# Optimization experiments

Measured on AMD Instinct MI355X. Metric: run time of the kernel, lower is better.

The kernel has to match this reference:

```python
import jax, jax.numpy as jnp
import numpy as np

WS = 7          # window_size
NH = 12         # num_heads
EPS = 1e-5      # LayerNorm eps


def setup_inputs() -> dict:
    key = jax.random.key(0)
    ks = jax.random.split(key, 8)
    B, H, W, C = 32, 56, 56, 384
    x = jax.random.normal(ks[0], (B, H * W, C), dtype=jnp.float32)
    s = 1.0 / np.sqrt(C)
    return {
        "x": x,
        "ln_gamma": jnp.ones((C,), jnp.float32),
        "ln_beta": jnp.zeros((C,), jnp.float32),
        "w_in": jax.random.normal(ks[1], (3 * C, C), jnp.float32) * s,   # torch in_proj_weight
        "b_in": jnp.zeros((3 * C,), jnp.float32),
        "w_out": jax.random.normal(ks[2], (C, C), jnp.float32) * s,      # torch out_proj.weight
        "b_out": jnp.zeros((C,), jnp.float32),
        "H": H,
        "W": W,
    }


def reference(x, ln_gamma, ln_beta, w_in, b_in, w_out, b_out, H, W):
    B, N, C = x.shape
    assert N == H * W
    hd = C // NH
    shortcut = x

    # LayerNorm
    mu = jnp.mean(x, axis=-1, keepdims=True)
    var = jnp.mean((x - mu) ** 2, axis=-1, keepdims=True)
    y = (x - mu) * jax.lax.rsqrt(var + EPS) * ln_gamma + ln_beta

    # window partition (pads are static Python ints)
    y = y.reshape(B, H, W, C)
    pad_h = (WS - H % WS) % WS
    pad_w = (WS - W % WS) % WS
    y = jnp.pad(y, ((0, 0), (0, pad_h), (0, pad_w), (0, 0)))
    Hp, Wp = H + pad_h, W + pad_w
    nh, nw = Hp // WS, Wp // WS
    y = y.reshape(B, nh, WS, nw, WS, C).transpose(0, 1, 3, 2, 4, 5)
    y = y.reshape(B * nh * nw, WS * WS, C)   # [NWIN, L, C]

    # MHA (torch nn.MultiheadAttention, batch_first)
    qkv = y @ w_in.T + b_in                   # [NWIN, L, 3C]
    q, k, v = jnp.split(qkv, 3, axis=-1)
    NWIN, L, _ = y.shape
    q = q.reshape(NWIN, L, NH, hd).transpose(0, 2, 1, 3)
    k = k.reshape(NWIN, L, NH, hd).transpose(0, 2, 1, 3)
    v = v.reshape(NWIN, L, NH, hd).transpose(0, 2, 1, 3)
    scores = jnp.einsum("whqd,whkd->whqk", q, k) / jnp.sqrt(jnp.float32(hd))
    attn = jax.nn.softmax(scores, axis=-1)
    o = jnp.einsum("whqk,whkd->whqd", attn, v)
    o = o.transpose(0, 2, 1, 3).reshape(NWIN, L, C)
    o = o @ w_out.T + b_out

    # window reverse + unpad + residual
    o = o.reshape(B, nh, nw, WS, WS, C).transpose(0, 1, 3, 2, 4, 5)
    o = o.reshape(B, Hp, Wp, C)[:, :H, :W, :].reshape(B, N, C)
    return shortcut + o
```

## Files before the change

### kernel.cpp

```cpp
#include <hip/hip_runtime.h>

typedef __bf16 bf16x8 __attribute__((ext_vector_type(8)));
typedef float f32x4 __attribute__((ext_vector_type(4)));
typedef unsigned short ushort8 __attribute__((ext_vector_type(8)));
typedef unsigned int uu2 __attribute__((ext_vector_type(2)));

#define LDS_AS(p) ((__attribute__((address_space(3))) void*)(p))
#define GLB_AS(p) ((const __attribute__((address_space(1))) void*)(p))

__device__ __forceinline__ unsigned short f2bf(float f) {
    union { float f; unsigned u; } v; v.f = f;
    unsigned r = v.u + 0x7fffu + ((v.u >> 16) & 1u);
    return (unsigned short)(r >> 16);
}

__global__ __launch_bounds__(256) void convw_kernel(
    const float* __restrict__ wi, const float* __restrict__ wo,
    unsigned short* __restrict__ qw, unsigned short* __restrict__ ow)
{
    const int i = blockIdx.x * 256 + threadIdx.x;
    if (i < 1152 * 384) qw[i] = f2bf(wi[i]);
    if (i < 384 * 384)  ow[i] = f2bf(wo[i]);
}

__global__ __launch_bounds__(256) void ln_kernel(
    const float* __restrict__ x, const float* __restrict__ gam,
    const float* __restrict__ bet, unsigned short* __restrict__ y)
{
    const int lane = threadIdx.x & 63;
    const int wv   = threadIdx.x >> 6;
    const int m    = blockIdx.x * 4 + wv;
    const int win  = m / 49, l = m - win * 49;
    const int b = win >> 6, wh = (win >> 3) & 7, ww = win & 7;
    const int i = l / 7, j = l - i * 7;
    const float2* xr = (const float2*)(x + ((size_t)b * 3136 + (wh * 7 + i) * 56 + (ww * 7 + j)) * 384);

    float2 v[3];
    float s = 0.f, ss = 0.f;
#pragma unroll
    for (int t = 0; t < 3; ++t) {
        v[t] = xr[t * 64 + lane];
        s  += v[t].x + v[t].y;
        ss += v[t].x * v[t].x + v[t].y * v[t].y;
    }
#pragma unroll
    for (int d = 1; d < 64; d <<= 1) {
        s  += __shfl_xor(s, d, 64);
        ss += __shfl_xor(ss, d, 64);
    }
    const float mu  = s * (1.f / 384.f);
    const float var = ss * (1.f / 384.f) - mu * mu;
    const float rs  = rsqrtf(var + 1e-5f);

    unsigned* yr = (unsigned*)(y + (size_t)m * 384);
#pragma unroll
    for (int t = 0; t < 3; ++t) {
        const int c = (t * 64 + lane) * 2;
        float a0 = (v[t].x - mu) * rs * gam[c]     + bet[c];
        float a1 = (v[t].y - mu) * rs * gam[c + 1] + bet[c + 1];
        yr[t * 64 + lane] = (unsigned)f2bf(a0) | ((unsigned)f2bf(a1) << 16);
    }
}

template <int N_, int EPI>
__global__ __launch_bounds__(256) void gemm_kernel(
    const unsigned short* __restrict__ A,
    const unsigned short* __restrict__ Bw,
    const float* __restrict__ bias,
    unsigned short* __restrict__ obf,
    const float* __restrict__ xres,
    float* __restrict__ oflt)
{
    __shared__ unsigned short As[2][128 * 32];
    __shared__ unsigned short Bs[2][128 * 32];
    const int lane = threadIdx.x & 63;
    const int wv   = threadIdx.x >> 6;

    const int NB = N_ / 128;
    int sw = blockIdx.x;
    if ((gridDim.x & 7) == 0)
        sw = (sw & 7) * (int)(gridDim.x >> 3) + (sw >> 3);
    const int my = sw / NB;
    const int m0 = my * 128;
    const int n0 = (sw - my * NB) * 128;

    const int wm = (wv & 1) * 64;
    const int wn = (wv >> 1) * 64;
    const int cl = lane & 15;
    const int qd = lane >> 4;
    const int srow = wv * 16 + (lane >> 2);
    const int scol = (lane & 3) * 8;

    f32x4 acc[4][4] = {};

#define STAGE(BUF, KB) do {                                                                              \
    const unsigned short* ga = A  + (size_t)(m0 + srow) * 384 + (KB) * 32 + scol;                        \
    const unsigned short* gb = Bw + (size_t)(n0 + srow) * 384 + (KB) * 32 + scol;                        \
    __builtin_amdgcn_global_load_lds(GLB_AS(ga),            LDS_AS(&As[BUF][(wv * 16) * 32]),        16, 0, 0); \
    __builtin_amdgcn_global_load_lds(GLB_AS(ga + 64 * 384), LDS_AS(&As[BUF][(64 + wv * 16) * 32]),   16, 0, 0); \
    __builtin_amdgcn_global_load_lds(GLB_AS(gb),            LDS_AS(&Bs[BUF][(wv * 16) * 32]),        16, 0, 0); \
    __builtin_amdgcn_global_load_lds(GLB_AS(gb + 64 * 384), LDS_AS(&Bs[BUF][(64 + wv * 16) * 32]),   16, 0, 0); \
  } while (0)

    STAGE(0, 0);
    __syncthreads();

#pragma unroll
    for (int kb = 0; kb < 12; ++kb) {
        const int cur = kb & 1;
        if (kb < 11) STAGE(cur ^ 1, kb + 1);

        bf16x8 af[4], bfr[4];
#pragma unroll
        for (int mt = 0; mt < 4; ++mt)
            af[mt] = *(const bf16x8*)(&As[cur][(wm + mt * 16 + cl) * 32 + qd * 8]);
#pragma unroll
        for (int nt = 0; nt < 4; ++nt)
            bfr[nt] = *(const bf16x8*)(&Bs[cur][(wn + nt * 16 + cl) * 32 + qd * 8]);
#pragma unroll
        for (int mt = 0; mt < 4; ++mt)
#pragma unroll
            for (int nt = 0; nt < 4; ++nt)
                acc[mt][nt] = __builtin_amdgcn_mfma_f32_16x16x32_bf16(bfr[nt], af[mt], acc[mt][nt], 0, 0, 0);

        __syncthreads();
    }
#undef STAGE

#pragma unroll
    for (int mt = 0; mt < 4; ++mt) {
        const int m = m0 + wm + mt * 16 + cl;
        size_t rowbase = 0;
        if (EPI == 1) {
            const int win = m / 49, l = m - win * 49;
            const int b = win >> 6, wh = (win >> 3) & 7, ww = win & 7;
            const int i = l / 7, j = l - i * 7;
            rowbase = ((size_t)b * 3136 + (wh * 7 + i) * 56 + (ww * 7 + j)) * 384;
        }
#pragma unroll
        for (int nt = 0; nt < 4; ++nt) {
            const int nb = n0 + wn + nt * 16 + qd * 4;
            const f32x4 bv = *(const f32x4*)(bias + nb);
            if (EPI == 0) {
                uu2 p;
                p[0] = (unsigned)f2bf(acc[mt][nt][0] + bv[0]) |
                       ((unsigned)f2bf(acc[mt][nt][1] + bv[1]) << 16);
                p[1] = (unsigned)f2bf(acc[mt][nt][2] + bv[2]) |
                       ((unsigned)f2bf(acc[mt][nt][3] + bv[3]) << 16);
                *(uu2*)(obf + (size_t)m * N_ + nb) = p;
            } else {
                const f32x4 xr = *(const f32x4*)(xres + rowbase + nb);
                f32x4 o;
#pragma unroll
                for (int r = 0; r < 4; ++r) o[r] = acc[mt][nt][r] + bv[r] + xr[r];
                *(f32x4*)(oflt + rowbase + nb) = o;
            }
        }
    }
}

__global__ __launch_bounds__(256) void attn_kernel(
    const unsigned short* __restrict__ qkv, unsigned short* __restrict__ o)
{
    __shared__ unsigned short P[4][64 * 72];
    const int lane = threadIdx.x & 63;
    const int wv   = threadIdx.x >> 6;
    const int cl = lane & 15;
    const int qd = lane >> 4;
    const int g   = blockIdx.x * 4 + wv;
    const int win = g / 12;
    const int h   = g - win * 12;
    const unsigned short* base = qkv + (size_t)win * (49 * 1152);

    bf16x8 aq[4], bk[4];
#pragma unroll
    for (int mt = 0; mt < 4; ++mt) {
        const int l = mt * 16 + cl;
        bf16x8 z = {};
        if (l < 49) z = *(const bf16x8*)(base + (size_t)l * 1152 + h * 32 + qd * 8);
        aq[mt] = z;
    }
#pragma unroll
    for (int nt = 0; nt < 4; ++nt) {
        const int lk = nt * 16 + cl;
        bf16x8 z = {};
        if (lk < 49) z = *(const bf16x8*)(base + (size_t)lk * 1152 + 384 + h * 32 + qd * 8);
        bk[nt] = z;
    }
    f32x4 s[4][4] = {};
#pragma unroll
    for (int mt = 0; mt < 4; ++mt)
#pragma unroll
        for (int nt = 0; nt < 4; ++nt)
            s[mt][nt] = __builtin_amdgcn_mfma_f32_16x16x32_bf16(aq[mt], bk[nt], s[mt][nt], 0, 0, 0);

    const float scale = 0.17677669529663687f;
#pragma unroll
    for (int mt = 0; mt < 4; ++mt)
#pragma unroll
        for (int nt = 0; nt < 4; ++nt)
#pragma unroll
            for (int r = 0; r < 4; ++r) {
                float t = s[mt][nt][r] * scale;
                if (nt * 16 + cl >= 49) t = -1e30f;
                s[mt][nt][r] = t;
            }

#pragma unroll
    for (int mt = 0; mt < 4; ++mt)
#pragma unroll
        for (int r = 0; r < 4; ++r) {
            float mx = fmaxf(fmaxf(s[mt][0][r], s[mt][1][r]), fmaxf(s[mt][2][r], s[mt][3][r]));
            mx = fmaxf(mx, __shfl_xor(mx, 1, 64));
            mx = fmaxf(mx, __shfl_xor(mx, 2, 64));
            mx = fmaxf(mx, __shfl_xor(mx, 4, 64));
            mx = fmaxf(mx, __shfl_xor(mx, 8, 64));
            float sm = 0.f;
#pragma unroll
            for (int nt = 0; nt < 4; ++nt) {
                const float p = __expf(s[mt][nt][r] - mx);
                s[mt][nt][r] = p;
                sm += p;
            }
            sm += __shfl_xor(sm, 1, 64);
            sm += __shfl_xor(sm, 2, 64);
            sm += __shfl_xor(sm, 4, 64);
            sm += __shfl_xor(sm, 8, 64);
            const float inv = 1.f / sm;
#pragma unroll
            for (int nt = 0; nt < 4; ++nt)
                s[mt][nt][r] *= inv;
        }

    unsigned short* Pw = &P[wv][0];
#pragma unroll
    for (int mt = 0; mt < 4; ++mt)
#pragma unroll
        for (int nt = 0; nt < 4; ++nt)
#pragma unroll
            for (int r = 0; r < 4; ++r)
                Pw[(mt * 16 + qd * 4 + r) * 72 + nt * 16 + cl] = f2bf(s[mt][nt][r]);

    f32x4 oa[4][2] = {};
    const unsigned short* vbase = base + 768 + h * 32;
#pragma unroll
    for (int kk = 0; kk < 2; ++kk) {
        bf16x8 ap[4];
#pragma unroll
        for (int mt = 0; mt < 4; ++mt)
            ap[mt] = *(const bf16x8*)(Pw + (mt * 16 + cl) * 72 + kk * 32 + qd * 8);
#pragma unroll
        for (int nt = 0; nt < 2; ++nt) {
            ushort8 tv;
#pragma unroll
            for (int jj = 0; jj < 8; ++jj) {
                const int lk = kk * 32 + qd * 8 + jj;
                tv[jj] = (lk < 49) ? vbase[(size_t)lk * 1152 + nt * 16 + cl] : (unsigned short)0;
            }
            const bf16x8 bv = __builtin_bit_cast(bf16x8, tv);
#pragma unroll
            for (int mt = 0; mt < 4; ++mt)
                oa[mt][nt] = __builtin_amdgcn_mfma_f32_16x16x32_bf16(ap[mt], bv, oa[mt][nt], 0, 0, 0);
        }
    }

    unsigned short* ob = o + (size_t)win * 49 * 384 + h * 32;
#pragma unroll
    for (int mt = 0; mt < 4; ++mt)
#pragma unroll
        for (int r = 0; r < 4; ++r) {
            const int l = mt * 16 + qd * 4 + r;
            if (l < 49) {
#pragma unroll
                for (int nt = 0; nt < 2; ++nt)
                    ob[(size_t)l * 384 + nt * 16 + cl] = f2bf(oa[mt][nt][r]);
            }
        }
}

extern "C" void kernel_launch(void* const* d_in, const int* in_sizes, int n_in,
                              void* d_out, int out_size, void* d_ws, size_t ws_size,
                              hipStream_t stream)
{
    const float* x   = (const float*)d_in[0];
    const float* gam = (const float*)d_in[1];
    const float* bet = (const float*)d_in[2];
    const float* wi  = (const float*)d_in[3];
    const float* bi  = (const float*)d_in[4];
    const float* wo  = (const float*)d_in[5];
    const float* bo  = (const float*)d_in[6];
    float* out = (float*)d_out;

    const int Bb   = in_sizes[0] / (3136 * 384);
    const int M    = Bb * 3136;
    const int NWIN = Bb * 64;

    char* ws = (char*)d_ws;
    unsigned short* qw   = (unsigned short*)(ws);
    unsigned short* ow   = (unsigned short*)(ws + 884736);
    unsigned short* y    = (unsigned short*)(ws + 1179648);
    unsigned short* qkv  = (unsigned short*)(ws + 1179648 + (size_t)M * 768);
    unsigned short* owin = (unsigned short*)(ws + 1179648 + (size_t)M * 768 + (size_t)M * 2304);

    convw_kernel<<<1728, 256, 0, stream>>>(wi, wo, qw, ow);
    ln_kernel<<<M / 4, 256, 0, stream>>>(x, gam, bet, y);
    gemm_kernel<1152, 0><<<(M / 128) * 9, 256, 0, stream>>>(y, qw, bi, qkv, nullptr, nullptr);
    attn_kernel<<<NWIN * 12 / 4, 256, 0, stream>>>(qkv, owin);
    gemm_kernel<384, 1><<<(M / 128) * 3, 256, 0, stream>>>(owin, ow, bo, nullptr, x, out);
}
```

Before: 646.5 us.

## Restructure GEMM into 256x128 tiles with 8 waves, K=64 stages and XOR-swizzled LDS

The GEMM block tile grows to 256x128 with 512 threads (8 waves) and K-step 64, and LDS is XOR-swizzled to avoid bank conflicts. Global-to-LDS loads for the next stage are split across four sub-phases, interleaved with MFMA groups, and separated by manual s_waitcnt/s_barrier plus setprio hints. The aim is better overlap of memory and compute and fewer barriers per unit of K. In exchange the kernel uses more LDS and more registers, and the hand-written waitcnt counts risk races if the compiler reorders memory operations. It also assumes M is divisible by 256; M = 100352 = 392*256, so that holds here.

Result: slower. 696.4 us (+7.7%).

```diff
diff --git a/kernel.cpp b/kernel.cpp
--- a/kernel.cpp
+++ b/kernel.cpp
@@ -63,7 +63,7 @@
 }
 
 template <int N_, int EPI>
-__global__ __launch_bounds__(256) void gemm_kernel(
+__global__ __launch_bounds__(512, 2) void gemm_kernel(
     const unsigned short* __restrict__ A,
     const unsigned short* __restrict__ Bw,
     const float* __restrict__ bias,
@@ -71,8 +71,8 @@
     const float* __restrict__ xres,
     float* __restrict__ oflt)
 {
-    __shared__ unsigned short As[2][128 * 32];
-    __shared__ unsigned short Bs[2][128 * 32];
+    __shared__ unsigned short As[2][256 * 64];
+    __shared__ unsigned short Bs[2][128 * 64];
     const int lane = threadIdx.x & 63;
     const int wv   = threadIdx.x >> 6;
 
@@ -81,51 +81,100 @@
     if ((gridDim.x & 7) == 0)
         sw = (sw & 7) * (int)(gridDim.x >> 3) + (sw >> 3);
     const int my = sw / NB;
-    const int m0 = my * 128;
+    const int m0 = my * 256;
     const int n0 = (sw - my * NB) * 128;
 
-    const int wm = (wv & 1) * 64;
-    const int wn = (wv >> 1) * 64;
+    const int wm = (wv & 3) * 64;
+    const int wn = (wv >> 2) * 64;
     const int cl = lane & 15;
     const int qd = lane >> 4;
-    const int srow = wv * 16 + (lane >> 2);
-    const int scol = (lane & 3) * 8;
+    const int rc0 = ((qd ^ (cl & 7)) * 8);
+
+    const int srow  = lane >> 3;
+    const int sperm = ((lane & 7) ^ srow) * 8;
+
+    const unsigned short* gA = A  + (size_t)(m0 + wv * 32 + srow) * 384 + sperm;
+    const unsigned short* gB = Bw + (size_t)(n0 + wv * 16 + srow) * 384 + sperm;
 
     f32x4 acc[4][4] = {};
 
-#define STAGE(BUF, KB) do {                                                                              \
-    const unsigned short* ga = A  + (size_t)(m0 + srow) * 384 + (KB) * 32 + scol;                        \
-    const unsigned short* gb = Bw + (size_t)(n0 + srow) * 384 + (KB) * 32 + scol;                        \
-    __builtin_amdgcn_global_load_lds(GLB_AS(ga),            LDS_AS(&As[BUF][(wv * 16) * 32]),        16, 0, 0); \
-    __builtin_amdgcn_global_load_lds(GLB_AS(ga + 64 * 384), LDS_AS(&As[BUF][(64 + wv * 16) * 32]),   16, 0, 0); \
-    __builtin_amdgcn_global_load_lds(GLB_AS(gb),            LDS_AS(&Bs[BUF][(wv * 16) * 32]),        16, 0, 0); \
-    __builtin_amdgcn_global_load_lds(GLB_AS(gb + 64 * 384), LDS_AS(&Bs[BUF][(64 + wv * 16) * 32]),   16, 0, 0); \
-  } while (0)
-
-    STAGE(0, 0);
-    __syncthreads();
-
-#pragma unroll
-    for (int kb = 0; kb < 12; ++kb) {
+#define GLA(BUF, KT, I) __builtin_amdgcn_global_load_lds(GLB_AS(gA + (I) * 8 * 384 + (KT) * 64), \
+                            LDS_AS(&As[BUF][(wv * 32 + (I) * 8) * 64]), 16, 0, 0)
+#define GLB_(BUF, KT, I) __builtin_amdgcn_global_load_lds(GLB_AS(gB + (I) * 8 * 384 + (KT) * 64), \
+                            LDS_AS(&Bs[BUF][(wv * 16 + (I) * 8) * 64]), 16, 0, 0)
+#define LDA(row, off) (*(const bf16x8*)(Ac + (row) * 64 + (off)))
+#define LDB(row, off) (*(const bf16x8*)(Bc + (row) * 64 + (off)))
+
+    GLA(0, 0, 0); GLA(0, 0, 1); GLA(0, 0, 2); GLA(0, 0, 3);
+    GLB_(0, 0, 0); GLB_(0, 0, 1);
+
+#pragma unroll
+    for (int kb = 0; kb < 6; ++kb) {
         const int cur = kb & 1;
-        if (kb < 11) STAGE(cur ^ 1, kb + 1);
-
-        bf16x8 af[4], bfr[4];
-#pragma unroll
-        for (int mt = 0; mt < 4; ++mt)
-            af[mt] = *(const bf16x8*)(&As[cur][(wm + mt * 16 + cl) * 32 + qd * 8]);
-#pragma unroll
-        for (int nt = 0; nt < 4; ++nt)
-            bfr[nt] = *(const bf16x8*)(&Bs[cur][(wn + nt * 16 + cl) * 32 + qd * 8]);
-#pragma unroll
-        for (int mt = 0; mt < 4; ++mt)
-#pragma unroll
-            for (int nt = 0; nt < 4; ++nt)
-                acc[mt][nt] = __builtin_amdgcn_mfma_f32_16x16x32_bf16(bfr[nt], af[mt], acc[mt][nt], 0, 0, 0);
-
-        __syncthreads();
-    }
-#undef STAGE
+        const int nxt = cur ^ 1;
+
+        if (kb < 5) {
+            GLA(nxt, kb + 1, 0); GLA(nxt, kb + 1, 1);
+            asm volatile("s_waitcnt vmcnt(2)\n\ts_barrier" ::: "memory");
+        } else {
+            asm volatile("s_waitcnt vmcnt(0)\n\ts_barrier" ::: "memory");
+        }
+
+        const unsigned short* Ac = &As[cur][0];
+        const unsigned short* Bc = &Bs[cur][0];
+        const int rc1 = rc0 ^ 32;
+        bf16x8 af0, af1, bf[4];
+
+        af0 = LDA(wm + cl,      rc0);
+        af1 = LDA(wm + 16 + cl, rc0);
+#pragma unroll
+        for (int nt = 0; nt < 4; ++nt) bf[nt] = LDB(wn + nt * 16 + cl, rc0);
+        __builtin_amdgcn_s_setprio(1);
+#pragma unroll
+        for (int nt = 0; nt < 4; ++nt) acc[0][nt] = __builtin_amdgcn_mfma_f32_16x16x32_bf16(bf[nt], af0, acc[0][nt], 0, 0, 0);
+#pragma unroll
+        for (int nt = 0; nt < 4; ++nt) acc[1][nt] = __builtin_amdgcn_mfma_f32_16x16x32_bf16(bf[nt], af1, acc[1][nt], 0, 0, 0);
+        __builtin_amdgcn_s_setprio(0);
+        asm volatile("s_barrier" ::: "memory");
+
+        af0 = LDA(wm + 32 + cl, rc0);
+        af1 = LDA(wm + 48 + cl, rc0);
+        if (kb < 5) { GLA(nxt, kb + 1, 2); GLA(nxt, kb + 1, 3); }
+        __builtin_amdgcn_s_setprio(1);
+#pragma unroll
+        for (int nt = 0; nt < 4; ++nt) acc[2][nt] = __builtin_amdgcn_mfma_f32_16x16x32_bf16(bf[nt], af0, acc[2][nt], 0, 0, 0);
+#pragma unroll
+        for (int nt = 0; nt < 4; ++nt) acc[3][nt] = __builtin_amdgcn_mfma_f32_16x16x32_bf16(bf[nt], af1, acc[3][nt], 0, 0, 0);
+        __builtin_amdgcn_s_setprio(0);
+        asm volatile("s_barrier" ::: "memory");
+
+        af0 = LDA(wm + cl,      rc1);
+        af1 = LDA(wm + 16 + cl, rc1);
+#pragma unroll
+        for (int nt = 0; nt < 4; ++nt) bf[nt] = LDB(wn + nt * 16 + cl, rc1);
+        if (kb < 5) { GLB_(nxt, kb + 1, 0); GLB_(nxt, kb + 1, 1); }
+        __builtin_amdgcn_s_setprio(1);
+#pragma unroll
+        for (int nt = 0; nt < 4; ++nt) acc[0][nt] = __builtin_amdgcn_mfma_f32_16x16x32_bf16(bf[nt], af0, acc[0][nt], 0, 0, 0);
+#pragma unroll
+        for (int nt = 0; nt < 4; ++nt) acc[1][nt] = __builtin_amdgcn_mfma_f32_16x16x32_bf16(bf[nt], af1, acc[1][nt], 0, 0, 0);
+        __builtin_amdgcn_s_setprio(0);
+        asm volatile("s_barrier" ::: "memory");
+
+        af0 = LDA(wm + 32 + cl, rc1);
+        af1 = LDA(wm + 48 + cl, rc1);
+        __builtin_amdgcn_s_setprio(1);
+#pragma unroll
+        for (int nt = 0; nt < 4; ++nt) acc[2][nt] = __builtin_amdgcn_mfma_f32_16x16x32_bf16(bf[nt], af0, acc[2][nt], 0, 0, 0);
+#pragma unroll
+        for (int nt = 0; nt < 4; ++nt) acc[3][nt] = __builtin_amdgcn_mfma_f32_16x16x32_bf16(bf[nt], af1, acc[3][nt], 0, 0, 0);
+        __builtin_amdgcn_s_setprio(0);
+        asm volatile("s_barrier" ::: "memory");
+    }
+#undef GLA
+#undef GLB_
+#undef LDA
+#undef LDB
 
 #pragma unroll
     for (int mt = 0; mt < 4; ++mt) {
@@ -304,7 +353,7 @@
 
     convw_kernel<<<1728, 256, 0, stream>>>(wi, wo, qw, ow);
     ln_kernel<<<M / 4, 256, 0, stream>>>(x, gam, bet, y);
-    gemm_kernel<1152, 0><<<(M / 128) * 9, 256, 0, stream>>>(y, qw, bi, qkv, nullptr, nullptr);
+    gemm_kernel<1152, 0><<<(M / 256) * 9, 512, 0, stream>>>(y, qw, bi, qkv, nullptr, nullptr);
     attn_kernel<<<NWIN * 12 / 4, 256, 0, stream>>>(qkv, owin);
-    gemm_kernel<384, 1><<<(M / 128) * 3, 256, 0, stream>>>(owin, ow, bo, nullptr, x, out);
-}
+    gemm_kernel<384, 1><<<(M / 256) * 3, 512, 0, stream>>>(owin, ow, bo, nullptr, x, out);
+}
```
